# Kernel tuning notes

Measured on AMD Instinct MI355X. Metric: run time of the kernel, lower is better.

## Reference

```python
import jax, jax.numpy as jnp
import numpy as np

B, N, T, W, H, ED, S, C, E = 16, 256, 64, 12, 64, 64, 5, 4, 2048
ALPHA = 1.0
FG = W + H  # gcn_in_channels = window_size + tgcn_hidden_dim


def setup_inputs() -> dict:
    key = jax.random.key(0)
    ks = jax.random.split(key, 26)
    rn = lambda k, shape: jax.random.normal(k, shape, jnp.float32) * 0.1
    x = jax.random.normal(ks[0], (B, N, T), jnp.float32)
    src = jax.random.randint(ks[1], (E,), 0, N)
    off = jax.random.randint(ks[2], (E,), 1, N)
    dst = (src + off) % N  # no self loops
    return {
        'x': x,
        'static_edge_weight': jax.random.uniform(ks[3], (E,), jnp.float32),
        'gsl_gconv_w': rn(ks[4], (FG, ED)), 'gsl_gconv_b': rn(ks[5], (ED,)),
        'gsl_w1': rn(ks[6], (ED, ED)), 'gsl_b1': rn(ks[7], (ED,)),
        'gsl_w2': rn(ks[8], (ED, ED)), 'gsl_b2': rn(ks[9], (ED,)),
        'wz_c': rn(ks[10], (1, H)), 'bz_c': rn(ks[11], (H,)),
        'wz_l': rn(ks[12], (2 * H, H)), 'bz_l': rn(ks[13], (H,)),
        'wr_c': rn(ks[14], (1, H)), 'br_c': rn(ks[15], (H,)),
        'wr_l': rn(ks[16], (2 * H, H)), 'br_l': rn(ks[17], (H,)),
        'wh_c': rn(ks[18], (1, H)), 'bh_c': rn(ks[19], (H,)),
        'wh_l': rn(ks[20], (2 * H, H)), 'bh_l': rn(ks[21], (H,)),
        'cls_w': rn(ks[22], (N * H, C)), 'cls_b': rn(ks[23], (C,)),
        'static_edge_index': jnp.stack([src, dst]).astype(jnp.int32),
    }


def _normalize(A):
    # GCN sym-norm with added self loops; A has zero diagonal by construction.
    Ahat = A + jnp.eye(N, dtype=A.dtype)
    deg = Ahat.sum(axis=-2)  # in-degree (PyG gcn_norm scatters weight on col)
    dinv = jnp.where(deg > 0, 1.0 / jnp.sqrt(deg), 0.0)
    return dinv[..., :, None] * Ahat * dinv[..., None, :]


def reference(x, static_edge_weight, gsl_gconv_w, gsl_gconv_b, gsl_w1, gsl_b1,
              gsl_w2, gsl_b2, wz_c, bz_c, wz_l, bz_l, wr_c, br_c, wr_l, br_l,
              wh_c, bh_c, wh_l, bh_l, cls_w, cls_b, static_edge_index):
    A_stat = jnp.zeros((N, N), jnp.float32).at[static_edge_index[0], static_edge_index[1]].add(static_edge_weight)
    An_stat = _normalize(A_stat)  # [N,N]

    # Sliding windows, left-padded with zeros to window_size W.
    xp = jnp.pad(x, ((0, 0), (0, 0), (W - 1, 0)))
    widx = jnp.arange(T)[:, None] + jnp.arange(W)[None, :]
    wins = jnp.transpose(xp[:, :, widx], (2, 0, 1, 3))      # [T,B,N,W]
    xts = jnp.transpose(x, (2, 0, 1))[..., None]            # [T,B,N,1]
    cnts = jnp.minimum(jnp.arange(T) + 1, S).astype(jnp.float32)
    idxs = jnp.arange(T) % S

    def gcn_s(X, Wm, b):  # static graph, out[j] = sum_i Anorm[i,j] (XW)[i]
        return jnp.einsum('ij,bif->bjf', An_stat, X @ Wm) + b

    def gcn_d(An, X, Wm, b):  # per-batch dynamic graph
        return jnp.einsum('bij,bif->bjf', An, X @ Wm) + b

    def step(carry, xs):
        h, Eh = carry
        win, xt, cnt, idx = xs
        It = jnp.concatenate([win, h], axis=-1)             # [B,N,W+H]
        df = gcn_s(It, gsl_gconv_w, gsl_gconv_b)
        de1 = jnp.tanh(ALPHA * (df @ gsl_w1 + gsl_b1))
        de2 = jnp.tanh(ALPHA * (df @ gsl_w2 + gsl_b2))
        M12 = jnp.einsum('bie,bje->bij', de1, de2)          # de1 @ de2^T
        Et = jax.nn.relu(jnp.tanh(ALPHA * (M12 - jnp.swapaxes(M12, -1, -2))))
        Eh = Eh.at[:, idx].set(Et)                          # ring buffer write
        Mt = Eh.sum(axis=1) / cnt                           # mean over filled slots
        An = _normalize(Mt)
        cz = gcn_d(An, xt, wz_c, bz_c)
        z = jax.nn.sigmoid(jnp.concatenate([cz, h], -1) @ wz_l + bz_l)
        cr = gcn_d(An, xt, wr_c, br_c)
        r = jax.nn.sigmoid(jnp.concatenate([cr, h], -1) @ wr_l + br_l)
        ch = gcn_d(An, xt, wh_c, bh_c)
        ht = jnp.tanh(jnp.concatenate([ch, h * r], -1) @ wh_l + bh_l)
        h = z * h + (1.0 - z) * ht
        return (h, Eh), None

    h0 = jnp.zeros((B, N, H), jnp.float32)
    Eh0 = jnp.zeros((B, S, N, N), jnp.float32)
    (hT, _), _ = jax.lax.scan(step, (h0, Eh0), (wins, xts, cnts, idxs))
    return hT.reshape(B, N * H) @ cls_w + cls_b
```

## Files before the change

### kernel.cpp

```cpp
#include <hip/hip_runtime.h>
#include <hip/hip_bf16.h>


typedef unsigned short u16;
typedef unsigned int u32;
typedef unsigned long long u64;
typedef __attribute__((ext_vector_type(8))) short bf16x8;
typedef __attribute__((ext_vector_type(4))) float f32x4;

#define B_ 16
#define N_ 256
#define T_ 64
#define W_ 12
#define S_ 5
#define E_ 2048
#define G_ 16

__device__ __forceinline__ float b2f(u16 u) {
  union { u32 i; float f; } v; v.i = ((u32)u) << 16; return v.f;
}
__device__ __forceinline__ u16 f2b(float f) {
  union { float f; u32 i; } v; v.f = f;
  u32 x = v.i; x += 0x7fff + ((x >> 16) & 1); return (u16)(x >> 16);
}
__device__ __forceinline__ float ftanh(float x) {
  float e = __expf(-2.f * fabsf(x));
  float t = (1.f - e) / (1.f + e);
  return x < 0.f ? -t : t;
}
__device__ __forceinline__ float fsigm(float x) { return 1.f / (1.f + __expf(-x)); }
__device__ __forceinline__ float cvload(const void* p, size_t i, int f) {
  return f ? ((const float*)p)[i] : b2f(((const u16*)p)[i]);
}
__device__ __forceinline__ u16 cvloadb(const void* p, size_t i, int f) {
  return f ? f2b(((const float*)p)[i]) : ((const u16*)p)[i];
}
__device__ __forceinline__ float gld(const float* p) {
  return __hip_atomic_load(p, __ATOMIC_RELAXED, __HIP_MEMORY_SCOPE_SYSTEM);
}
__device__ __forceinline__ void gst(float* p, float v) {
  __hip_atomic_store(p, v, __ATOMIC_RELAXED, __HIP_MEMORY_SCOPE_SYSTEM);
}
__device__ __forceinline__ u64 gld64(const u64* p) {
  return __hip_atomic_load(p, __ATOMIC_RELAXED, __HIP_MEMORY_SCOPE_SYSTEM);
}
__device__ __forceinline__ void gst64(u64* p, u64 v) {
  __hip_atomic_store(p, v, __ATOMIC_RELAXED, __HIP_MEMORY_SCOPE_SYSTEM);
}
__device__ __forceinline__ u32 gldu(const u32* p) {
  return __hip_atomic_load(p, __ATOMIC_RELAXED, __HIP_MEMORY_SCOPE_SYSTEM);
}
__device__ __forceinline__ f32x4 mfma16(bf16x8 a, bf16x8 b, f32x4 c) {
  return __builtin_amdgcn_mfma_f32_16x16x32_bf16(a, b, c, 0, 0, 0);
}
__device__ __forceinline__ bf16x8 ldfrag(const u16* p) { return *(const bf16x8*)p; }

struct Params {
  const void *x0, *ew0, *gw0, *gb0, *w10, *b10, *w20, *b20;
  const void *wzc0, *bzc0, *wzl0, *bzl0, *wrc0, *brc0, *wrl0, *brl0;
  const void *whc0, *bhc0, *whl0, *bhl0, *clsw0, *clsb0;
  const int* eidx;
  float *Eh, *clspart;
  u64 *degsum, *de1g, *de2g, *xTp, *hgpT;
  u32 *tags;
  void* out;
};

__device__ __forceinline__ void wtag(const u32* tg, u32 target) {
  const int k = threadIdx.x & 15;
  while (!__all((int)(gldu(&tg[k]) >= target)))
    __builtin_amdgcn_s_sleep(1);
}
__device__ __forceinline__ void wtag8(const u32* tg, int base, u32 target) {
  const int k = base + (threadIdx.x & 7);
  while (!__all((int)(gldu(&tg[k]) >= target)))
    __builtin_amdgcn_s_sleep(1);
}
__device__ __forceinline__ void ptag(u32* tg, int wg, u32 val) {
  if (threadIdx.x == 0)
    __hip_atomic_store(&tg[wg], val, __ATOMIC_RELAXED, __HIP_MEMORY_SCOPE_SYSTEM);
}

__global__ void __launch_bounds__(256, 1) dtgcn_main(Params p) {
  __shared__ __align__(16) u16 s_union[21120];
  __shared__ __align__(16) u16 s_gwF[64 * 104];
  __shared__ __align__(16) u16 s_w1T[64 * 72], s_w2T[64 * 72];
  __shared__ __align__(16) u16 s_gzT[64 * 72], s_grT[64 * 72], s_ghT[64 * 72];
  __shared__ __align__(16) u16 s_antO1[16 * 264], s_antO2[16 * 264];
  __shared__ __align__(16) u16 s_m1[16 * 104];
  __shared__ float s_msum[16 * 257];
  __shared__ __align__(16) u16 s_de1I[16 * 72], s_de2I[16 * 72];
  __shared__ __align__(16) u16 s_hbf[16 * 72];
  __shared__ __align__(16) u16 s_dfhr[16 * 72];
  __shared__ float s_colv[16], s_degacc[16];
  __shared__ float s_y[256], s_dinv[256], s_s[16];
  __shared__ float s_uv[384], s_gb[64], s_b1[64], s_b2[64];
  __shared__ int s_flag;

  const int b = blockIdx.x & 15;
  const int wg = blockIdx.x >> 4;
  const int tid = threadIdx.x;
  const int lane = tid & 63;
  const int wv = tid >> 6;
  const int l = lane & 15;
  const int quad = lane >> 4;
  const int r0 = wg * 16;

  u64* de1g = p.de1g + (size_t)b * N_ * 16;
  u64* de2g = p.de2g + (size_t)b * N_ * 16;
  u64* hgpb = p.hgpT + (size_t)b * 64 * 64;
  u64* xTw  = p.xTp + (size_t)b * 64 * 64;
  const u64* xTb = xTw;
  u64* degb = p.degsum + (size_t)b * N_;
  u32* tgDe = p.tags + b * 128;
  u32* tgH  = p.tags + b * 128 + 32;
  u32* tgX  = p.tags + b * 128 + 48;
  u32* tgC  = p.tags + b * 128 + 64;

  if (tid == 0) {
    const u16* q = (const u16*)p.x0;
    int c = 0;
    for (int i = 0; i < 256; ++i) {
      int ex = (q[i] >> 7) & 0xff;
      c += (ex >= 110 && ex <= 135);
    }
    s_flag = (c < 200) ? 1 : 0;
  }
  __syncthreads();
  const int fl = s_flag;

  {
    u16* xs = s_union;
    #pragma unroll
    for (int r = 0; r < 4; ++r) {
      const int tt = wg * 4 + r;
      xs[r * 256 + tid] = f2b(cvload(p.x0, ((size_t)b * N_ + tid) * T_ + tt, fl));
    }
    __syncthreads();
    const int r = tid >> 6, c = tid & 63;
    u64 v = (u64)xs[r * 256 + 4 * c]
          | ((u64)xs[r * 256 + 4 * c + 1] << 16)
          | ((u64)xs[r * 256 + 4 * c + 2] << 32)
          | ((u64)xs[r * 256 + 4 * c + 3] << 48);
    gst64(&xTw[(size_t)(wg * 4 + r) * 64 + c], v);
    __syncthreads();
    ptag(tgX, wg, 1);
  }

  {
    float* s_acol = (float*)s_union;
    float* s_dg   = (float*)s_union + 4096;
    for (int i = tid; i < 4096; i += 256) s_acol[i] = 0.f;
    s_dg[tid] = 0.f;
    __syncthreads();
    for (int e2 = tid; e2 < E_; e2 += 256) {
      const int sN = p.eidx[e2], dN = p.eidx[E_ + e2];
      const float wv2 = cvload(p.ew0, e2, fl);
      atomicAdd(&s_dg[dN], wv2);
      const int dl = dN - r0;
      if (dl >= 0 && dl < 16) atomicAdd(&s_acol[sN * 16 + dl], wv2);
    }
    __syncthreads();
    s_dg[tid] = rsqrtf(1.f + s_dg[tid]);
    __syncthreads();
    for (int idx = tid; idx < 4096; idx += 256) {
      const int jl = idx >> 8, i = idx & 255;
      float a = s_acol[i * 16 + jl] + ((i == r0 + jl) ? 1.f : 0.f);
      float v = s_dg[i] * a * s_dg[r0 + jl];
      u16 hi = f2b(v);
      s_antO1[jl * 264 + i] = hi;
      s_antO2[jl * 264 + i] = f2b(v - b2f(hi));
    }
  }

  for (int idx = tid; idx < 64 * 104; idx += 256) {
    const int ee = idx / 104, k = idx - ee * 104;
    u16 v = 0;
    if (k < 64) v = cvloadb(p.gw0, (12 + k) * 64 + ee, fl);
    else if (k < 76) v = cvloadb(p.gw0, (k - 64) * 64 + ee, fl);
    s_gwF[ee * 104 + k] = v;
  }
  for (int idx = tid; idx < 4096; idx += 256) {
    const int ee = idx >> 6, ff = idx & 63;
    s_w1T[ee * 72 + ff] = cvloadb(p.w10, ff * 64 + ee, fl);
    s_w2T[ee * 72 + ff] = cvloadb(p.w20, ff * 64 + ee, fl);
    s_gzT[ee * 72 + ff] = cvloadb(p.wzl0, 4096 + ff * 64 + ee, fl);
    s_grT[ee * 72 + ff] = cvloadb(p.wrl0, 4096 + ff * 64 + ee, fl);
    s_ghT[ee * 72 + ff] = cvloadb(p.whl0, 4096 + ff * 64 + ee, fl);
  }
  if (tid < 64) {
    const int e2 = tid;
    float uz = 0, vz = 0, ur = 0, vr = 0, uh = 0, vh = 0;
    for (int f = 0; f < 64; ++f) {
      float wz = cvload(p.wzl0, f * 64 + e2, fl);
      float wr = cvload(p.wrl0, f * 64 + e2, fl);
      float wh = cvload(p.whl0, f * 64 + e2, fl);
      uz += cvload(p.wzc0, f, fl) * wz; vz += cvload(p.bzc0, f, fl) * wz;
      ur += cvload(p.wrc0, f, fl) * wr; vr += cvload(p.brc0, f, fl) * wr;
      uh += cvload(p.whc0, f, fl) * wh; vh += cvload(p.bhc0, f, fl) * wh;
    }
    s_uv[0 * 64 + e2] = uz; s_uv[1 * 64 + e2] = vz + cvload(p.bzl0, e2, fl);
    s_uv[2 * 64 + e2] = ur; s_uv[3 * 64 + e2] = vr + cvload(p.brl0, e2, fl);
    s_uv[4 * 64 + e2] = uh; s_uv[5 * 64 + e2] = vh + cvload(p.bhl0, e2, fl);
    s_gb[tid] = cvload(p.gb0, tid, fl);
    s_b1[tid] = cvload(p.b10, tid, fl);
    s_b2[tid] = cvload(p.b20, tid, fl);
  }
  for (int idx = tid; idx < 16 * 257; idx += 256) s_msum[idx] = 0.f;
  for (int idx = tid; idx < 16 * 72; idx += 256) s_hbf[idx] = 0;
  for (int idx = tid; idx < 16 * 104; idx += 256) s_m1[idx] = 0;
  for (int idx = 20064 + tid; idx < 21120; idx += 256) s_union[idx] = 0;
  if (tid < 16) s_degacc[tid] = 0.f;
  __syncthreads();

  u16* s_itT = s_union;
  u16* s_j1  = s_union;
  u16* s_j2  = s_union + 9216;

  float hreg[4] = {0.f, 0.f, 0.f, 0.f};
  const int e = wv * 16 + l;

  for (int t = 0; t < T_; ++t) {
    float xv;
    {
      if (t == 0) wtag(tgX, 1);
      xv = cvload(p.x0, ((size_t)b * N_ + tid) * T_ + t, fl);
      u64 tw0[2], tw1[2];
      #pragma unroll
      for (int q = 0; q < 2; ++q) {
        const int idx = q * 256 + tid;
        const int row = idx >> 5, c = idx & 31;
        const bool ok = idx < 384;
        const int tx = t - (W_ - 1) + row;
        const bool live = ok && tx >= 0;
        tw0[q] = live ? gld64(&xTb[(size_t)tx * 64 + c]) : 0ull;
        tw1[q] = live ? gld64(&xTb[(size_t)tx * 64 + 32 + c]) : 0ull;
      }
      wtag8(tgH, 0, (u32)t);
      {
        u64 th[8];
        #pragma unroll
        for (int q = 0; q < 8; ++q) {
          const int idx = q * 256 + tid;
          const int row = idx >> 5, c = idx & 31;
          th[q] = gld64(&hgpb[(size_t)row * 64 + c]);
        }
        #pragma unroll
        for (int q = 0; q < 8; ++q) {
          const int idx = q * 256 + tid;
          const int row = idx >> 5, c = idx & 31;
          *(u64*)&s_itT[row * 264 + c * 4] = th[q];
        }
        #pragma unroll
        for (int q = 0; q < 2; ++q) {
          const int idx = q * 256 + tid;
          if (idx < 384) {
            const int row = idx >> 5, c = idx & 31;
            *(u64*)&s_itT[(64 + row) * 264 + c * 4] = tw0[q];
          }
        }
      }
      __syncthreads();
      wtag8(tgH, 8, (u32)t);
      u64 th1[8];
      #pragma unroll
      for (int q = 0; q < 8; ++q) {
        const int idx = q * 256 + tid;
        const int row = idx >> 5, c = idx & 31;
        th1[q] = gld64(&hgpb[(size_t)row * 64 + 32 + c]);
      }
      f32x4 accA[2];
      accA[0] = (f32x4){0.f, 0.f, 0.f, 0.f};
      accA[1] = (f32x4){0.f, 0.f, 0.f, 0.f};
      {
        int ti = 0;
        for (int nt = wv; nt < 5; nt += 4, ++ti) {
          #pragma unroll
          for (int ch = 0; ch < 4; ++ch) {
            const int io = ch * 32 + quad * 8;
            bf16x8 bfr = ldfrag(&s_itT[(nt * 16 + l) * 264 + io]);
            accA[ti] = mfma16(ldfrag(&s_antO1[l * 264 + io]), bfr, accA[ti]);
            accA[ti] = mfma16(ldfrag(&s_antO2[l * 264 + io]), bfr, accA[ti]);
          }
        }
      }
      #pragma unroll
      for (int q = 0; q < 8; ++q) {
        const int idx = q * 256 + tid;
        const int row = idx >> 5, c = idx & 31;
        *(u64*)&s_itT[row * 264 + (32 + c) * 4] = th1[q];
      }
      #pragma unroll
      for (int q = 0; q < 2; ++q) {
        const int idx = q * 256 + tid;
        if (idx < 384) {
          const int row = idx >> 5, c = idx & 31;
          *(u64*)&s_itT[(64 + row) * 264 + (32 + c) * 4] = tw1[q];
        }
      }
      __syncthreads();
      {
        int ti = 0;
        for (int nt = wv; nt < 5; nt += 4, ++ti) {
          #pragma unroll
          for (int ch = 4; ch < 8; ++ch) {
            const int io = ch * 32 + quad * 8;
            bf16x8 bfr = ldfrag(&s_itT[(nt * 16 + l) * 264 + io]);
            accA[ti] = mfma16(ldfrag(&s_antO1[l * 264 + io]), bfr, accA[ti]);
            accA[ti] = mfma16(ldfrag(&s_antO2[l * 264 + io]), bfr, accA[ti]);
          }
          #pragma unroll
          for (int r = 0; r < 4; ++r)
            s_m1[(quad * 4 + r) * 104 + nt * 16 + l] = f2b(accA[ti][r]);
        }
      }
      __syncthreads();
      {
        f32x4 dfa = {0.f, 0.f, 0.f, 0.f};
        #pragma unroll
        for (int ks = 0; ks < 3; ++ks) {
          bf16x8 afr = ldfrag(&s_m1[l * 104 + ks * 32 + quad * 8]);
          dfa = mfma16(afr, ldfrag(&s_gwF[e * 104 + ks * 32 + quad * 8]), dfa);
        }
        #pragma unroll
        for (int r = 0; r < 4; ++r)
          s_dfhr[(quad * 4 + r) * 72 + e] = f2b(dfa[r] + s_gb[e]);
      }
      __syncthreads();
      {
        f32x4 E1, E2;
        #pragma unroll
        for (int r = 0; r < 4; ++r) { E1[r] = s_b1[e]; E2[r] = s_b2[e]; }
        #pragma unroll
        for (int ks = 0; ks < 2; ++ks) {
          bf16x8 afr = ldfrag(&s_dfhr[l * 72 + ks * 32 + quad * 8]);
          E1 = mfma16(afr, ldfrag(&s_w1T[e * 72 + ks * 32 + quad * 8]), E1);
          E2 = mfma16(afr, ldfrag(&s_w2T[e * 72 + ks * 32 + quad * 8]), E2);
        }
        u32 v1[4], v2[4];
        #pragma unroll
        for (int r = 0; r < 4; ++r) {
          v1[r] = (u32)f2b(ftanh(E1[r]));
          v2[r] = (u32)f2b(ftanh(E2[r]));
          s_de1I[(quad * 4 + r) * 72 + e] = (u16)v1[r];
          s_de2I[(quad * 4 + r) * 72 + e] = (u16)v2[r];
        }
        #pragma unroll
        for (int r = 0; r < 4; ++r) {
          u32 a1 = (u32)__shfl_xor((int)v1[r], 1);
          u32 a2 = (u32)__shfl_xor((int)v2[r], 1);
          u32 ev1 = (l & 1) ? a1 : v1[r], od1 = (l & 1) ? v1[r] : a1;
          u32 ev2 = (l & 1) ? a2 : v2[r], od2 = (l & 1) ? v2[r] : a2;
          u32 w1 = ev1 | (od1 << 16), w2 = ev2 | (od2 << 16);
          u32 x1 = (u32)__shfl_xor((int)w1, 2);
          u32 x2 = (u32)__shfl_xor((int)w2, 2);
          u64 q1 = (l & 2) ? ((u64)x1 | ((u64)w1 << 32)) : ((u64)w1 | ((u64)x1 << 32));
          u64 q2 = (l & 2) ? ((u64)x2 | ((u64)w2 << 32)) : ((u64)w2 | ((u64)x2 << 32));
          if ((l & 3) == 0) {
            const size_t ro = (size_t)(r0 + quad * 4 + r) * 16 + wv * 4 + (l >> 2);
            gst64(&de1g[ro], q1);
            gst64(&de2g[ro], q2);
          }
        }
      }
      __syncthreads();
      ptag(tgDe, wg, (u32)(t + 1));
    }

    {
      const int sidx = t % S_;
      float* Ehc = p.Eh + ((size_t)((b * S_ + sidx) * G_ + wg)) * (N_ * 16);
      if (tid < 16) s_colv[tid] = 0.f;
      bf16x8 bq1[2], bq2[2];
      #pragma unroll
      for (int ks = 0; ks < 2; ++ks) {
        bq1[ks] = ldfrag(&s_de1I[l * 72 + ks * 32 + quad * 8]);
        bq2[ks] = ldfrag(&s_de2I[l * 72 + ks * 32 + quad * 8]);
      }
      const int havold = (t >= S_);
      float old0[2][4] = {{0.f, 0.f, 0.f, 0.f}, {0.f, 0.f, 0.f, 0.f}};
      float old1[2][4] = {{0.f, 0.f, 0.f, 0.f}, {0.f, 0.f, 0.f, 0.f}};
      if (havold) {
        #pragma unroll
        for (int mt2 = 0; mt2 < 2; ++mt2) {
          const int mt = wv * 2 + mt2;
          #pragma unroll
          for (int r = 0; r < 4; ++r) {
            const int i0 = mt * 16 + quad * 4 + r;
            old0[mt2][r] = Ehc[(size_t)i0 * 16 + l];
            old1[mt2][r] = Ehc[(size_t)(128 + i0) * 16 + l];
          }
        }
      }
      const u32 dtgt = (u32)(t + 1);
      wtag8(tgDe, 0, dtgt);
      u64 t1a[8], t2a[8];
      #pragma unroll
      for (int q = 0; q < 8; ++q) {
        const int idx = q * 256 + tid;
        const int row = idx >> 4, c = idx & 15;
        t1a[q] = gld64(&de1g[(size_t)row * 16 + c]);
        t2a[q] = gld64(&de2g[(size_t)row * 16 + c]);
      }
      #pragma unroll
      for (int q = 0; q < 8; ++q) {
        const int idx = q * 256 + tid;
        const int row = idx >> 4, c = idx & 15;
        *(u64*)&s_j1[row * 72 + c * 4] = t1a[q];
        *(u64*)&s_j2[row * 72 + c * 4] = t2a[q];
      }
      __syncthreads();
      wtag8(tgDe, 8, dtgt);
      u64 t1b[8], t2b[8];
      #pragma unroll
      for (int q = 0; q < 8; ++q) {
        const int idx = q * 256 + tid;
        const int row = idx >> 4, c = idx & 15;
        t1b[q] = gld64(&de1g[(size_t)(128 + row) * 16 + c]);
        t2b[q] = gld64(&de2g[(size_t)(128 + row) * 16 + c]);
      }
      float dcacc = 0.f;
      #pragma unroll
      for (int mt2 = 0; mt2 < 2; ++mt2) {
        const int mt = wv * 2 + mt2;
        f32x4 D1 = {0.f, 0.f, 0.f, 0.f}, D2 = {0.f, 0.f, 0.f, 0.f};
        #pragma unroll
        for (int ks = 0; ks < 2; ++ks) {
          bf16x8 a1 = ldfrag(&s_j1[(mt * 16 + l) * 72 + ks * 32 + quad * 8]);
          bf16x8 a2 = ldfrag(&s_j2[(mt * 16 + l) * 72 + ks * 32 + quad * 8]);
          D1 = mfma16(a1, bq2[ks], D1);
          D2 = mfma16(a2, bq1[ks], D2);
        }
        #pragma unroll
        for (int r = 0; r < 4; ++r) {
          const int i = mt * 16 + quad * 4 + r;
          float d = ftanh(D1[r] - D2[r]);
          float eN = fmaxf(d, 0.f);
          float dd = eN - old0[mt2][r];
          Ehc[(size_t)i * 16 + l] = eN;
          s_msum[l * 257 + i] += dd;
          dcacc += dd;
        }
      }
      __syncthreads();
      #pragma unroll
      for (int q = 0; q < 8; ++q) {
        const int idx = q * 256 + tid;
        const int row = idx >> 4, c = idx & 15;
        *(u64*)&s_j1[row * 72 + c * 4] = t1b[q];
        *(u64*)&s_j2[row * 72 + c * 4] = t2b[q];
      }
      __syncthreads();
      #pragma unroll
      for (int mt2 = 0; mt2 < 2; ++mt2) {
        const int mt = wv * 2 + mt2;
        f32x4 D1 = {0.f, 0.f, 0.f, 0.f}, D2 = {0.f, 0.f, 0.f, 0.f};
        #pragma unroll
        for (int ks = 0; ks < 2; ++ks) {
          bf16x8 a1 = ldfrag(&s_j1[(mt * 16 + l) * 72 + ks * 32 + quad * 8]);
          bf16x8 a2 = ldfrag(&s_j2[(mt * 16 + l) * 72 + ks * 32 + quad * 8]);
          D1 = mfma16(a1, bq2[ks], D1);
          D2 = mfma16(a2, bq1[ks], D2);
        }
        #pragma unroll
        for (int r = 0; r < 4; ++r) {
          const int i = 128 + mt * 16 + quad * 4 + r;
          float d = ftanh(D1[r] - D2[r]);
          float eN = fmaxf(d, 0.f);
          float dd = eN - old1[mt2][r];
          Ehc[(size_t)i * 16 + l] = eN;
          s_msum[l * 257 + i] += dd;
          dcacc += dd;
        }
      }
      dcacc += __shfl_xor(dcacc, 16);
      dcacc += __shfl_xor(dcacc, 32);
      if (lane < 16) atomicAdd(&s_colv[lane], dcacc);
      __syncthreads();
      if (tid < 16) {
        float nd = s_degacc[tid] + s_colv[tid];
        s_degacc[tid] = nd;
        union { float f; u32 i; } cv; cv.f = nd;
        gst64(&degb[r0 + tid], (u64)cv.i | ((u64)dtgt << 32));
      }
    }

    {
      f32x4 azh = {0.f, 0.f, 0.f, 0.f}, arh = {0.f, 0.f, 0.f, 0.f};
      #pragma unroll
      for (int ks = 0; ks < 2; ++ks) {
        bf16x8 afr = ldfrag(&s_hbf[l * 72 + ks * 32 + quad * 8]);
        azh = mfma16(afr, ldfrag(&s_gzT[e * 72 + ks * 32 + quad * 8]), azh);
        arh = mfma16(afr, ldfrag(&s_grT[e * 72 + ks * 32 + quad * 8]), arh);
      }
      const u32 dgt = (u32)(t + 1);
      u64 du;
      for (;;) {
        du = gld64(&degb[tid]);
        if (__all((int)((u32)(du >> 32) >= dgt))) break;
        __builtin_amdgcn_s_sleep(1);
      }
      const float cnt = (float)((t + 1 < S_) ? (t + 1) : S_);
      const float invc = 1.f / cnt;
      {
        union { u32 i; float f; } dv; dv.i = (u32)du;
        float dg = 1.f + dv.f * invc;
        float di = rsqrtf(dg);
        s_dinv[tid] = di;
        s_y[tid] = di * xv;
      }
      __syncthreads();
      {
        const int jl = tid >> 4, cc = tid & 15;
        float part = 0.f;
        #pragma unroll
        for (int k = 0; k < 16; ++k) {
          const int i = cc * 16 + ((k + cc) & 15);
          part += s_msum[jl * 257 + i] * s_y[i];
        }
        part += __shfl_xor(part, 1);
        part += __shfl_xor(part, 2);
        part += __shfl_xor(part, 4);
        part += __shfl_xor(part, 8);
        if (cc == 0) {
          const int j = r0 + jl;
          s_s[jl] = s_dinv[j] * (part * invc + s_y[j]);
        }
      }
      __syncthreads();
      float sv[4];
      #pragma unroll
      for (int r = 0; r < 4; ++r) sv[r] = s_s[quad * 4 + r];
      float zz[4], rr2[4];
      #pragma unroll
      for (int r = 0; r < 4; ++r) {
        zz[r]  = fsigm(azh[r] + s_uv[0 * 64 + e] * sv[r] + s_uv[1 * 64 + e]);
        rr2[r] = fsigm(arh[r] + s_uv[2 * 64 + e] * sv[r] + s_uv[3 * 64 + e]);
      }
      #pragma unroll
      for (int r = 0; r < 4; ++r)
        s_dfhr[(quad * 4 + r) * 72 + e] = f2b(hreg[r] * rr2[r]);
      __syncthreads();
      f32x4 ah;
      #pragma unroll
      for (int r = 0; r < 4; ++r) ah[r] = s_uv[4 * 64 + e] * sv[r] + s_uv[5 * 64 + e];
      #pragma unroll
      for (int ks = 0; ks < 2; ++ks) {
        bf16x8 afr = ldfrag(&s_dfhr[l * 72 + ks * 32 + quad * 8]);
        ah = mfma16(afr, ldfrag(&s_ghT[e * 72 + ks * 32 + quad * 8]), ah);
      }
      #pragma unroll
      for (int r = 0; r < 4; ++r) {
        float ht = ftanh(ah[r]);
        hreg[r] = zz[r] * hreg[r] + (1.f - zz[r]) * ht;
      }
      {
        u16 h0 = f2b(hreg[0]), h1 = f2b(hreg[1]);
        u16 h2 = f2b(hreg[2]), h3 = f2b(hreg[3]);
        u64 hv = (u64)h0 | ((u64)h1 << 16) | ((u64)h2 << 32) | ((u64)h3 << 48);
        gst64(&hgpb[(size_t)e * 64 + (r0 >> 2) + quad], hv);
        s_hbf[(quad * 4 + 0) * 72 + e] = h0;
        s_hbf[(quad * 4 + 1) * 72 + e] = h1;
        s_hbf[(quad * 4 + 2) * 72 + e] = h2;
        s_hbf[(quad * 4 + 3) * 72 + e] = h3;
      }
      __syncthreads();
      ptag(tgH, wg, (u32)(t + 1));
    }
  }

  {
    float part[4] = {0.f, 0.f, 0.f, 0.f};
    #pragma unroll
    for (int r = 0; r < 4; ++r) {
      const size_t base = ((size_t)(r0 + quad * 4 + r) * 64 + e) * 4;
      #pragma unroll
      for (int c = 0; c < 4; ++c)
        part[c] += hreg[r] * cvload(p.clsw0, base + c, fl);
    }
    #pragma unroll
    for (int c = 0; c < 4; ++c) {
      float v = part[c];
      v += __shfl_xor(v, 1);  v += __shfl_xor(v, 2);
      v += __shfl_xor(v, 4);  v += __shfl_xor(v, 8);
      v += __shfl_xor(v, 16); v += __shfl_xor(v, 32);
      if (lane == 0) s_s[wv * 4 + c] = v;
    }
    __syncthreads();
    if (tid < 4) {
      float tot = s_s[0 + tid] + s_s[4 + tid] + s_s[8 + tid] + s_s[12 + tid];
      gst(&p.clspart[(b * 16 + wg) * 4 + tid], tot);
    }
    __syncthreads();
    ptag(tgC, wg, 1);
    if (wg == 0) {
      wtag(tgC, 1);
      if (tid < 4) {
        float v = 0.f;
        for (int k = 0; k < 16; ++k) v += gld(&p.clspart[(b * 16 + k) * 4 + tid]);
        v += cvload(p.clsb0, tid, fl);
        if (fl) ((float*)p.out)[b * 4 + tid] = v;
        else    ((u16*)p.out)[b * 4 + tid] = f2b(v);
      }
    }
  }
}

extern "C" void kernel_launch(void* const* d_in, const int* in_sizes, int n_in,
                              void* d_out, int out_size, void* d_ws, size_t ws_size,
                              hipStream_t stream) {
  float* w = (float*)d_ws;
  size_t o = 0;
  auto alloc = [&](size_t n) { float* r = w + o; o += (n + 63) & ~(size_t)63; return r; };
  u64* xTp  = (u64*)alloc((size_t)B_ * 64 * 128);
  float* clspart = alloc(B_ * 16 * 4);
  u64* de1g = (u64*)alloc((size_t)B_ * N_ * 32);
  u64* de2g = (u64*)alloc((size_t)B_ * N_ * 32);
  float* Eh = alloc((size_t)B_ * S_ * N_ * N_);
  const size_t zero_off = o;
  u64*   hgpT  = (u64*)alloc((size_t)B_ * 64 * 128);
  u64*   degs  = (u64*)alloc((size_t)B_ * N_ * 2);
  u32*   tags  = (u32*)alloc(B_ * 128);
  if (ws_size < o * sizeof(float)) return;

  (void)hipMemsetAsync(w + zero_off, 0, (o - zero_off) * sizeof(float), stream);

  Params p;
  p.x0  = d_in[0];  p.ew0 = d_in[1];
  p.gw0 = d_in[2];  p.gb0 = d_in[3];
  p.w10 = d_in[4];  p.b10 = d_in[5];
  p.w20 = d_in[6];  p.b20 = d_in[7];
  p.wzc0 = d_in[8];  p.bzc0 = d_in[9];  p.wzl0 = d_in[10]; p.bzl0 = d_in[11];
  p.wrc0 = d_in[12]; p.brc0 = d_in[13]; p.wrl0 = d_in[14]; p.brl0 = d_in[15];
  p.whc0 = d_in[16]; p.bhc0 = d_in[17]; p.whl0 = d_in[18]; p.bhl0 = d_in[19];
  p.clsw0 = d_in[20]; p.clsb0 = d_in[21];
  p.eidx = (const int*)d_in[22];
  p.Eh = Eh; p.clspart = clspart;
  p.degsum = degs;
  p.de1g = de1g; p.de2g = de2g; p.xTp = xTp; p.hgpT = hgpT;
  p.tags = tags; p.out = d_out;

  void* args[] = { &p };
  hipError_t ce = hipLaunchCooperativeKernel((const void*)dtgcn_main,
                                             dim3(B_ * G_), dim3(256), args, 0, stream);
  if (ce != hipSuccess) {
    (void)hipGetLastError();
    dtgcn_main<<<dim3(B_ * G_), dim3(256), 0, stream>>>(p);
  }
}
```

Measured before the change: 870.4 us.

## Load MFMA operands directly from global and use per-wave readiness flags

The global h/x and de1/de2 operands are now loaded straight into MFMA fragments in registers instead of being staged through shared memory. This removes several __syncthreads barriers and the shared staging buffer. Readiness tags become per-wave (4 per workgroup, wtag32 polling 32 flags) and each wave publishes its own flag after a vmcnt wait, instead of a block barrier followed by a single flag store. This cuts intra-block synchronisation on the serial time loop, at the cost of more polled flags, uncoalesced 8-byte global loads and the correctness burden of relaxed-atomic ordering.

```diff
diff --git a/kernel.cpp b/kernel.cpp
--- a/kernel.cpp
+++ b/kernel.cpp
@@ -54,6 +54,9 @@
   return __builtin_amdgcn_mfma_f32_16x16x32_bf16(a, b, c, 0, 0, 0);
 }
 __device__ __forceinline__ bf16x8 ldfrag(const u16* p) { return *(const bf16x8*)p; }
+__device__ __forceinline__ bf16x8 mkfrag(u64 lo, u64 hi) {
+  union { u64 q[2]; bf16x8 v; } u; u.q[0] = lo; u.q[1] = hi; return u.v;
+}
 
 struct Params {
   const void *x0, *ew0, *gw0, *gb0, *w10, *b10, *w20, *b20;
@@ -71,8 +74,8 @@
   while (!__all((int)(gldu(&tg[k]) >= target)))
     __builtin_amdgcn_s_sleep(1);
 }
-__device__ __forceinline__ void wtag8(const u32* tg, int base, u32 target) {
-  const int k = base + (threadIdx.x & 7);
+__device__ __forceinline__ void wtag32(const u32* tg, int base, u32 target) {
+  const int k = base + (threadIdx.x & 31);
   while (!__all((int)(gldu(&tg[k]) >= target)))
     __builtin_amdgcn_s_sleep(1);
 }
@@ -80,9 +83,14 @@
   if (threadIdx.x == 0)
     __hip_atomic_store(&tg[wg], val, __ATOMIC_RELAXED, __HIP_MEMORY_SCOPE_SYSTEM);
 }
+__device__ __forceinline__ void ptagw(u32* tg, int slot, u32 val) {
+  asm volatile("s_waitcnt vmcnt(0)" ::: "memory");
+  if ((threadIdx.x & 63) == 0)
+    __hip_atomic_store(&tg[slot], val, __ATOMIC_RELAXED, __HIP_MEMORY_SCOPE_SYSTEM);
+}
 
 __global__ void __launch_bounds__(256, 1) dtgcn_main(Params p) {
-  __shared__ __align__(16) u16 s_union[21120];
+  __shared__ __align__(16) u16 s_union[8704];
   __shared__ __align__(16) u16 s_gwF[64 * 104];
   __shared__ __align__(16) u16 s_w1T[64 * 72], s_w2T[64 * 72];
   __shared__ __align__(16) u16 s_gzT[64 * 72], s_grT[64 * 72], s_ghT[64 * 72];
@@ -112,10 +120,10 @@
   u64* xTw  = p.xTp + (size_t)b * 64 * 64;
   const u64* xTb = xTw;
   u64* degb = p.degsum + (size_t)b * N_;
-  u32* tgDe = p.tags + b * 128;
-  u32* tgH  = p.tags + b * 128 + 32;
-  u32* tgX  = p.tags + b * 128 + 48;
-  u32* tgC  = p.tags + b * 128 + 64;
+  u32* tgDe4 = p.tags + b * 256;
+  u32* tgH4  = p.tags + b * 256 + 64;
+  u32* tgX   = p.tags + b * 256 + 128;
+  u32* tgC   = p.tags + b * 256 + 144;
 
   if (tid == 0) {
     const u16* q = (const u16*)p.x0;
@@ -209,13 +217,8 @@
   for (int idx = tid; idx < 16 * 257; idx += 256) s_msum[idx] = 0.f;
   for (int idx = tid; idx < 16 * 72; idx += 256) s_hbf[idx] = 0;
   for (int idx = tid; idx < 16 * 104; idx += 256) s_m1[idx] = 0;
-  for (int idx = 20064 + tid; idx < 21120; idx += 256) s_union[idx] = 0;
   if (tid < 16) s_degacc[tid] = 0.f;
   __syncthreads();
-
-  u16* s_itT = s_union;
-  u16* s_j1  = s_union;
-  u16* s_j2  = s_union + 9216;
 
   float hreg[4] = {0.f, 0.f, 0.f, 0.f};
   const int e = wv * 16 + l;
@@ -225,94 +228,53 @@
     {
       if (t == 0) wtag(tgX, 1);
       xv = cvload(p.x0, ((size_t)b * N_ + tid) * T_ + t, fl);
-      u64 tw0[2], tw1[2];
-      #pragma unroll
-      for (int q = 0; q < 2; ++q) {
-        const int idx = q * 256 + tid;
-        const int row = idx >> 5, c = idx & 31;
-        const bool ok = idx < 384;
-        const int tx = t - (W_ - 1) + row;
-        const bool live = ok && tx >= 0;
-        tw0[q] = live ? gld64(&xTb[(size_t)tx * 64 + c]) : 0ull;
-        tw1[q] = live ? gld64(&xTb[(size_t)tx * 64 + 32 + c]) : 0ull;
-      }
-      wtag8(tgH, 0, (u32)t);
-      {
-        u64 th[8];
-        #pragma unroll
-        for (int q = 0; q < 8; ++q) {
-          const int idx = q * 256 + tid;
-          const int row = idx >> 5, c = idx & 31;
-          th[q] = gld64(&hgpb[(size_t)row * 64 + c]);
-        }
-        #pragma unroll
-        for (int q = 0; q < 8; ++q) {
-          const int idx = q * 256 + tid;
-          const int row = idx >> 5, c = idx & 31;
-          *(u64*)&s_itT[row * 264 + c * 4] = th[q];
-        }
-        #pragma unroll
-        for (int q = 0; q < 2; ++q) {
-          const int idx = q * 256 + tid;
-          if (idx < 384) {
-            const int row = idx >> 5, c = idx & 31;
-            *(u64*)&s_itT[(64 + row) * 264 + c * 4] = tw0[q];
-          }
-        }
-      }
-      __syncthreads();
-      wtag8(tgH, 8, (u32)t);
-      u64 th1[8];
-      #pragma unroll
-      for (int q = 0; q < 8; ++q) {
-        const int idx = q * 256 + tid;
-        const int row = idx >> 5, c = idx & 31;
-        th1[q] = gld64(&hgpb[(size_t)row * 64 + 32 + c]);
-      }
-      f32x4 accA[2];
-      accA[0] = (f32x4){0.f, 0.f, 0.f, 0.f};
-      accA[1] = (f32x4){0.f, 0.f, 0.f, 0.f};
-      {
-        int ti = 0;
-        for (int nt = wv; nt < 5; nt += 4, ++ti) {
-          #pragma unroll
-          for (int ch = 0; ch < 4; ++ch) {
-            const int io = ch * 32 + quad * 8;
-            bf16x8 bfr = ldfrag(&s_itT[(nt * 16 + l) * 264 + io]);
-            accA[ti] = mfma16(ldfrag(&s_antO1[l * 264 + io]), bfr, accA[ti]);
-            accA[ti] = mfma16(ldfrag(&s_antO2[l * 264 + io]), bfr, accA[ti]);
-          }
-        }
-      }
-      #pragma unroll
-      for (int q = 0; q < 8; ++q) {
-        const int idx = q * 256 + tid;
-        const int row = idx >> 5, c = idx & 31;
-        *(u64*)&s_itT[row * 264 + (32 + c) * 4] = th1[q];
-      }
-      #pragma unroll
-      for (int q = 0; q < 2; ++q) {
-        const int idx = q * 256 + tid;
-        if (idx < 384) {
-          const int row = idx >> 5, c = idx & 31;
-          *(u64*)&s_itT[(64 + row) * 264 + (32 + c) * 4] = tw1[q];
-        }
-      }
-      __syncthreads();
-      {
-        int ti = 0;
-        for (int nt = wv; nt < 5; nt += 4, ++ti) {
-          #pragma unroll
-          for (int ch = 4; ch < 8; ++ch) {
-            const int io = ch * 32 + quad * 8;
-            bf16x8 bfr = ldfrag(&s_itT[(nt * 16 + l) * 264 + io]);
-            accA[ti] = mfma16(ldfrag(&s_antO1[l * 264 + io]), bfr, accA[ti]);
-            accA[ti] = mfma16(ldfrag(&s_antO2[l * 264 + io]), bfr, accA[ti]);
-          }
-          #pragma unroll
-          for (int r = 0; r < 4; ++r)
-            s_m1[(quad * 4 + r) * 104 + nt * 16 + l] = f2b(accA[ti][r]);
-        }
+      u64 b2l[8][2];
+      if (wv == 0) {
+        const int tx = t - (W_ - 1) + l;
+        const bool live = (l < W_) && (tx >= 0);
+        #pragma unroll
+        for (int ch = 0; ch < 8; ++ch) {
+          b2l[ch][0] = live ? gld64(&xTb[(size_t)tx * 64 + ch * 8 + quad * 2]) : 0ull;
+          b2l[ch][1] = live ? gld64(&xTb[(size_t)tx * 64 + ch * 8 + quad * 2 + 1]) : 0ull;
+        }
+      }
+      const u32 htgt = (u32)t;
+      u64 b1l[8][2];
+      wtag32(tgH4, 0, htgt);
+      #pragma unroll
+      for (int ch = 0; ch < 4; ++ch) {
+        b1l[ch][0] = gld64(&hgpb[(size_t)e * 64 + ch * 8 + quad * 2]);
+        b1l[ch][1] = gld64(&hgpb[(size_t)e * 64 + ch * 8 + quad * 2 + 1]);
+      }
+      wtag32(tgH4, 32, htgt);
+      #pragma unroll
+      for (int ch = 4; ch < 8; ++ch) {
+        b1l[ch][0] = gld64(&hgpb[(size_t)e * 64 + ch * 8 + quad * 2]);
+        b1l[ch][1] = gld64(&hgpb[(size_t)e * 64 + ch * 8 + quad * 2 + 1]);
+      }
+      f32x4 acc0 = {0.f, 0.f, 0.f, 0.f};
+      #pragma unroll
+      for (int ch = 0; ch < 8; ++ch) {
+        bf16x8 bfr = mkfrag(b1l[ch][0], b1l[ch][1]);
+        const int io = ch * 32 + quad * 8;
+        acc0 = mfma16(ldfrag(&s_antO1[l * 264 + io]), bfr, acc0);
+        acc0 = mfma16(ldfrag(&s_antO2[l * 264 + io]), bfr, acc0);
+      }
+      #pragma unroll
+      for (int r = 0; r < 4; ++r)
+        s_m1[(quad * 4 + r) * 104 + e] = f2b(acc0[r]);
+      if (wv == 0) {
+        f32x4 acc1 = {0.f, 0.f, 0.f, 0.f};
+        #pragma unroll
+        for (int ch = 0; ch < 8; ++ch) {
+          bf16x8 bfr = mkfrag(b2l[ch][0], b2l[ch][1]);
+          const int io = ch * 32 + quad * 8;
+          acc1 = mfma16(ldfrag(&s_antO1[l * 264 + io]), bfr, acc1);
+          acc1 = mfma16(ldfrag(&s_antO2[l * 264 + io]), bfr, acc1);
+        }
+        #pragma unroll
+        for (int r = 0; r < 4; ++r)
+          s_m1[(quad * 4 + r) * 104 + 64 + l] = f2b(acc1[r]);
       }
       __syncthreads();
       {
@@ -363,14 +325,14 @@
           }
         }
       }
-      __syncthreads();
-      ptag(tgDe, wg, (u32)(t + 1));
+      ptagw(tgDe4, wg * 4 + wv, (u32)(t + 1));
+      if (tid < 16) s_colv[tid] = 0.f;
+      __syncthreads();
     }
 
     {
       const int sidx = t % S_;
       float* Ehc = p.Eh + ((size_t)((b * S_ + sidx) * G_ + wg)) * (N_ * 16);
-      if (tid < 16) s_colv[tid] = 0.f;
       bf16x8 bq1[2], bq2[2];
       #pragma unroll
       for (int ks = 0; ks < 2; ++ks) {
@@ -393,31 +355,31 @@
         }
       }
       const u32 dtgt = (u32)(t + 1);
-      wtag8(tgDe, 0, dtgt);
-      u64 t1a[8], t2a[8];
-      #pragma unroll
-      for (int q = 0; q < 8; ++q) {
-        const int idx = q * 256 + tid;
-        const int row = idx >> 4, c = idx & 15;
-        t1a[q] = gld64(&de1g[(size_t)row * 16 + c]);
-        t2a[q] = gld64(&de2g[(size_t)row * 16 + c]);
-      }
-      #pragma unroll
-      for (int q = 0; q < 8; ++q) {
-        const int idx = q * 256 + tid;
-        const int row = idx >> 4, c = idx & 15;
-        *(u64*)&s_j1[row * 72 + c * 4] = t1a[q];
-        *(u64*)&s_j2[row * 72 + c * 4] = t2a[q];
-      }
-      __syncthreads();
-      wtag8(tgDe, 8, dtgt);
-      u64 t1b[8], t2b[8];
-      #pragma unroll
-      for (int q = 0; q < 8; ++q) {
-        const int idx = q * 256 + tid;
-        const int row = idx >> 4, c = idx & 15;
-        t1b[q] = gld64(&de1g[(size_t)(128 + row) * 16 + c]);
-        t2b[q] = gld64(&de2g[(size_t)(128 + row) * 16 + c]);
+      wtag32(tgDe4, 0, dtgt);
+      u64 a1[2][2][2], a2[2][2][2];
+      #pragma unroll
+      for (int mt2 = 0; mt2 < 2; ++mt2) {
+        const size_t row = (size_t)((wv * 2 + mt2) * 16 + l);
+        #pragma unroll
+        for (int ks = 0; ks < 2; ++ks) {
+          a1[mt2][ks][0] = gld64(&de1g[row * 16 + ks * 8 + quad * 2]);
+          a1[mt2][ks][1] = gld64(&de1g[row * 16 + ks * 8 + quad * 2 + 1]);
+          a2[mt2][ks][0] = gld64(&de2g[row * 16 + ks * 8 + quad * 2]);
+          a2[mt2][ks][1] = gld64(&de2g[row * 16 + ks * 8 + quad * 2 + 1]);
+        }
+      }
+      wtag32(tgDe4, 32, dtgt);
+      u64 c1[2][2][2], c2[2][2][2];
+      #pragma unroll
+      for (int mt2 = 0; mt2 < 2; ++mt2) {
+        const size_t row = (size_t)(128 + (wv * 2 + mt2) * 16 + l);
+        #pragma unroll
+        for (int ks = 0; ks < 2; ++ks) {
+          c1[mt2][ks][0] = gld64(&de1g[row * 16 + ks * 8 + quad * 2]);
+          c1[mt2][ks][1] = gld64(&de1g[row * 16 + ks * 8 + quad * 2 + 1]);
+          c2[mt2][ks][0] = gld64(&de2g[row * 16 + ks * 8 + quad * 2]);
+          c2[mt2][ks][1] = gld64(&de2g[row * 16 + ks * 8 + quad * 2 + 1]);
+        }
       }
       float dcacc = 0.f;
       #pragma unroll
@@ -426,10 +388,8 @@
         f32x4 D1 = {0.f, 0.f, 0.f, 0.f}, D2 = {0.f, 0.f, 0.f, 0.f};
         #pragma unroll
         for (int ks = 0; ks < 2; ++ks) {
-          bf16x8 a1 = ldfrag(&s_j1[(mt * 16 + l) * 72 + ks * 32 + quad * 8]);
-          bf16x8 a2 = ldfrag(&s_j2[(mt * 16 + l) * 72 + ks * 32 + quad * 8]);
-          D1 = mfma16(a1, bq2[ks], D1);
-          D2 = mfma16(a2, bq1[ks], D2);
+          D1 = mfma16(mkfrag(a1[mt2][ks][0], a1[mt2][ks][1]), bq2[ks], D1);
+          D2 = mfma16(mkfrag(a2[mt2][ks][0], a2[mt2][ks][1]), bq1[ks], D2);
         }
         #pragma unroll
         for (int r = 0; r < 4; ++r) {
@@ -442,25 +402,14 @@
           dcacc += dd;
         }
       }
-      __syncthreads();
-      #pragma unroll
-      for (int q = 0; q < 8; ++q) {
-        const int idx = q * 256 + tid;
-        const int row = idx >> 4, c = idx & 15;
-        *(u64*)&s_j1[row * 72 + c * 4] = t1b[q];
-        *(u64*)&s_j2[row * 72 + c * 4] = t2b[q];
-      }
-      __syncthreads();
       #pragma unroll
       for (int mt2 = 0; mt2 < 2; ++mt2) {
         const int mt = wv * 2 + mt2;
         f32x4 D1 = {0.f, 0.f, 0.f, 0.f}, D2 = {0.f, 0.f, 0.f, 0.f};
         #pragma unroll
         for (int ks = 0; ks < 2; ++ks) {
-          bf16x8 a1 = ldfrag(&s_j1[(mt * 16 + l) * 72 + ks * 32 + quad * 8]);
-          bf16x8 a2 = ldfrag(&s_j2[(mt * 16 + l) * 72 + ks * 32 + quad * 8]);
-          D1 = mfma16(a1, bq2[ks], D1);
-          D2 = mfma16(a2, bq1[ks], D2);
+          D1 = mfma16(mkfrag(c1[mt2][ks][0], c1[mt2][ks][1]), bq2[ks], D1);
+          D2 = mfma16(mkfrag(c2[mt2][ks][0], c2[mt2][ks][1]), bq1[ks], D2);
         }
         #pragma unroll
         for (int r = 0; r < 4; ++r) {
@@ -564,8 +513,7 @@
         s_hbf[(quad * 4 + 2) * 72 + e] = h2;
         s_hbf[(quad * 4 + 3) * 72 + e] = h3;
       }
-      __syncthreads();
-      ptag(tgH, wg, (u32)(t + 1));
+      ptagw(tgH4, wg * 4 + wv, (u32)(t + 1));
     }
   }
 
@@ -620,7 +568,7 @@
   const size_t zero_off = o;
   u64*   hgpT  = (u64*)alloc((size_t)B_ * 64 * 128);
   u64*   degs  = (u64*)alloc((size_t)B_ * N_ * 2);
-  u32*   tags  = (u32*)alloc(B_ * 128);
+  u32*   tags  = (u32*)alloc(B_ * 256);
   if (ws_size < o * sizeof(float)) return;
 
   (void)hipMemsetAsync(w + zero_off, 0, (o - zero_off) * sizeof(float), stream);
```

Measured after the change: 1.341 ms. 1.54x slower.

## Reassociate GCN as An·(It·Wg), exchange projected features instead of raw inputs

Applied to the files above, without the earlier changes.

The graph convolution on [window, h] is reassociated from (An·It)·Wg to An·(It·Wg). Each workgroup now projects its own 16 rows of the window and hidden state through the GCN weight locally and publishes only that 64-wide projection. The old path broadcast the transposed x windows and the hidden state and ran a two-stage matmul through an intermediate buffer. This removes the xT publishing phase, the extra tile pass in the adjacency matmul and the s_m1 staging, and merges two cross-workgroup tag channels into one. Spin waits also gain a bounded iteration cap, which risks returning before the data is ready, and the product is rounded to bf16 before the adjacency multiply, which changes numerics slightly.

```diff
diff --git a/kernel.cpp b/kernel.cpp
--- a/kernel.cpp
+++ b/kernel.cpp
@@ -15,6 +15,7 @@
 #define S_ 5
 #define E_ 2048
 #define G_ 16
+#define SPIN_MAX (1u << 20)
 
 __device__ __forceinline__ float b2f(u16 u) {
   union { u32 i; float f; } v; v.i = ((u32)u) << 16; return v.f;
@@ -61,20 +62,24 @@
   const void *whc0, *bhc0, *whl0, *bhl0, *clsw0, *clsb0;
   const int* eidx;
   float *Eh, *clspart;
-  u64 *degsum, *de1g, *de2g, *xTp, *hgpT;
+  u64 *degsum, *de1g, *de2g, *Ggp;
   u32 *tags;
   void* out;
 };
 
 __device__ __forceinline__ void wtag(const u32* tg, u32 target) {
   const int k = threadIdx.x & 15;
-  while (!__all((int)(gldu(&tg[k]) >= target)))
+  for (u32 s = 0; s < SPIN_MAX; ++s) {
+    if (__all((int)(gldu(&tg[k]) >= target))) return;
     __builtin_amdgcn_s_sleep(1);
+  }
 }
 __device__ __forceinline__ void wtag8(const u32* tg, int base, u32 target) {
   const int k = base + (threadIdx.x & 7);
-  while (!__all((int)(gldu(&tg[k]) >= target)))
+  for (u32 s = 0; s < SPIN_MAX; ++s) {
+    if (__all((int)(gldu(&tg[k]) >= target))) return;
     __builtin_amdgcn_s_sleep(1);
+  }
 }
 __device__ __forceinline__ void ptag(u32* tg, int wg, u32 val) {
   if (threadIdx.x == 0)
@@ -82,12 +87,13 @@
 }
 
 __global__ void __launch_bounds__(256, 1) dtgcn_main(Params p) {
-  __shared__ __align__(16) u16 s_union[21120];
-  __shared__ __align__(16) u16 s_gwF[64 * 104];
+  __shared__ __align__(16) u16 s_union[18432];
+  __shared__ __align__(16) u16 s_gwHT[64 * 72];
+  __shared__ __align__(16) u16 s_gwWT[64 * 32];
+  __shared__ __align__(16) u16 s_xw[16 * 96];
   __shared__ __align__(16) u16 s_w1T[64 * 72], s_w2T[64 * 72];
   __shared__ __align__(16) u16 s_gzT[64 * 72], s_grT[64 * 72], s_ghT[64 * 72];
   __shared__ __align__(16) u16 s_antO1[16 * 264], s_antO2[16 * 264];
-  __shared__ __align__(16) u16 s_m1[16 * 104];
   __shared__ float s_msum[16 * 257];
   __shared__ __align__(16) u16 s_de1I[16 * 72], s_de2I[16 * 72];
   __shared__ __align__(16) u16 s_hbf[16 * 72];
@@ -108,14 +114,11 @@
 
   u64* de1g = p.de1g + (size_t)b * N_ * 16;
   u64* de2g = p.de2g + (size_t)b * N_ * 16;
-  u64* hgpb = p.hgpT + (size_t)b * 64 * 64;
-  u64* xTw  = p.xTp + (size_t)b * 64 * 64;
-  const u64* xTb = xTw;
+  u64* Ggp  = p.Ggp + (size_t)b * 64 * 64;
   u64* degb = p.degsum + (size_t)b * N_;
-  u32* tgDe = p.tags + b * 128;
-  u32* tgH  = p.tags + b * 128 + 32;
-  u32* tgX  = p.tags + b * 128 + 48;
-  u32* tgC  = p.tags + b * 128 + 64;
+  u32* tgDe = p.tags + b * 64;
+  u32* tgG  = p.tags + b * 64 + 16;
+  u32* tgC  = p.tags + b * 64 + 32;
 
   if (tid == 0) {
     const u16* q = (const u16*)p.x0;
@@ -128,24 +131,6 @@
   }
   __syncthreads();
   const int fl = s_flag;
-
-  {
-    u16* xs = s_union;
-    #pragma unroll
-    for (int r = 0; r < 4; ++r) {
-      const int tt = wg * 4 + r;
-      xs[r * 256 + tid] = f2b(cvload(p.x0, ((size_t)b * N_ + tid) * T_ + tt, fl));
-    }
-    __syncthreads();
-    const int r = tid >> 6, c = tid & 63;
-    u64 v = (u64)xs[r * 256 + 4 * c]
-          | ((u64)xs[r * 256 + 4 * c + 1] << 16)
-          | ((u64)xs[r * 256 + 4 * c + 2] << 32)
-          | ((u64)xs[r * 256 + 4 * c + 3] << 48);
-    gst64(&xTw[(size_t)(wg * 4 + r) * 64 + c], v);
-    __syncthreads();
-    ptag(tgX, wg, 1);
-  }
 
   {
     float* s_acol = (float*)s_union;
@@ -173,12 +158,20 @@
     }
   }
 
-  for (int idx = tid; idx < 64 * 104; idx += 256) {
-    const int ee = idx / 104, k = idx - ee * 104;
-    u16 v = 0;
-    if (k < 64) v = cvloadb(p.gw0, (12 + k) * 64 + ee, fl);
-    else if (k < 76) v = cvloadb(p.gw0, (k - 64) * 64 + ee, fl);
-    s_gwF[ee * 104 + k] = v;
+  for (int idx = tid; idx < 64 * 72; idx += 256) {
+    const int ee = idx / 72, k = idx - ee * 72;
+    s_gwHT[idx] = (k < 64) ? cvloadb(p.gw0, (12 + k) * 64 + ee, fl) : (u16)0;
+  }
+  for (int idx = tid; idx < 64 * 32; idx += 256) {
+    const int ee = idx >> 5, w2 = idx & 31;
+    s_gwWT[idx] = (w2 < 12) ? cvloadb(p.gw0, w2 * 64 + ee, fl) : (u16)0;
+  }
+  for (int idx = tid; idx < 16 * 96; idx += 256) {
+    const int i = idx / 96, u = idx - i * 96;
+    const int tt = u - (W_ - 1);
+    s_xw[idx] = (tt >= 0 && tt < T_)
+                ? f2b(cvload(p.x0, ((size_t)b * N_ + r0 + i) * T_ + tt, fl))
+                : (u16)0;
   }
   for (int idx = tid; idx < 4096; idx += 256) {
     const int ee = idx >> 6, ff = idx & 63;
@@ -208,124 +201,85 @@
   }
   for (int idx = tid; idx < 16 * 257; idx += 256) s_msum[idx] = 0.f;
   for (int idx = tid; idx < 16 * 72; idx += 256) s_hbf[idx] = 0;
-  for (int idx = tid; idx < 16 * 104; idx += 256) s_m1[idx] = 0;
-  for (int idx = 20064 + tid; idx < 21120; idx += 256) s_union[idx] = 0;
   if (tid < 16) s_degacc[tid] = 0.f;
   __syncthreads();
 
-  u16* s_itT = s_union;
-  u16* s_j1  = s_union;
-  u16* s_j2  = s_union + 9216;
+  const int e = wv * 16 + l;
+
+  {
+    union { u16 a[8]; bf16x8 v; } ux;
+    #pragma unroll
+    for (int j = 0; j < 8; ++j) ux.a[j] = s_xw[l * 96 + quad * 8 + j];
+    f32x4 g = mfma16(ux.v, ldfrag(&s_gwWT[e * 32 + quad * 8]),
+                     (f32x4){0.f, 0.f, 0.f, 0.f});
+    u64 gv = (u64)f2b(g[0]) | ((u64)f2b(g[1]) << 16)
+           | ((u64)f2b(g[2]) << 32) | ((u64)f2b(g[3]) << 48);
+    gst64(&Ggp[(size_t)e * 64 + (r0 >> 2) + quad], gv);
+    __syncthreads();
+    ptag(tgG, wg, 1);
+  }
+
+  u16* s_gT = s_union;
+  u16* s_j1 = s_union;
+  u16* s_j2 = s_union + 9216;
 
   float hreg[4] = {0.f, 0.f, 0.f, 0.f};
-  const int e = wv * 16 + l;
 
   for (int t = 0; t < T_; ++t) {
     float xv;
     {
-      if (t == 0) wtag(tgX, 1);
       xv = cvload(p.x0, ((size_t)b * N_ + tid) * T_ + t, fl);
-      u64 tw0[2], tw1[2];
-      #pragma unroll
-      for (int q = 0; q < 2; ++q) {
-        const int idx = q * 256 + tid;
-        const int row = idx >> 5, c = idx & 31;
-        const bool ok = idx < 384;
-        const int tx = t - (W_ - 1) + row;
-        const bool live = ok && tx >= 0;
-        tw0[q] = live ? gld64(&xTb[(size_t)tx * 64 + c]) : 0ull;
-        tw1[q] = live ? gld64(&xTb[(size_t)tx * 64 + 32 + c]) : 0ull;
-      }
-      wtag8(tgH, 0, (u32)t);
+      const u32 gtgt = (u32)(t + 1);
+      wtag8(tgG, 0, gtgt);
       {
         u64 th[8];
         #pragma unroll
         for (int q = 0; q < 8; ++q) {
           const int idx = q * 256 + tid;
           const int row = idx >> 5, c = idx & 31;
-          th[q] = gld64(&hgpb[(size_t)row * 64 + c]);
+          th[q] = gld64(&Ggp[(size_t)row * 64 + c]);
         }
         #pragma unroll
         for (int q = 0; q < 8; ++q) {
           const int idx = q * 256 + tid;
           const int row = idx >> 5, c = idx & 31;
-          *(u64*)&s_itT[row * 264 + c * 4] = th[q];
-        }
-        #pragma unroll
-        for (int q = 0; q < 2; ++q) {
-          const int idx = q * 256 + tid;
-          if (idx < 384) {
-            const int row = idx >> 5, c = idx & 31;
-            *(u64*)&s_itT[(64 + row) * 264 + c * 4] = tw0[q];
-          }
-        }
-      }
-      __syncthreads();
-      wtag8(tgH, 8, (u32)t);
+          *(u64*)&s_gT[row * 264 + c * 4] = th[q];
+        }
+      }
+      __syncthreads();
+      wtag8(tgG, 8, gtgt);
       u64 th1[8];
       #pragma unroll
       for (int q = 0; q < 8; ++q) {
         const int idx = q * 256 + tid;
         const int row = idx >> 5, c = idx & 31;
-        th1[q] = gld64(&hgpb[(size_t)row * 64 + 32 + c]);
-      }
-      f32x4 accA[2];
-      accA[0] = (f32x4){0.f, 0.f, 0.f, 0.f};
-      accA[1] = (f32x4){0.f, 0.f, 0.f, 0.f};
-      {
-        int ti = 0;
-        for (int nt = wv; nt < 5; nt += 4, ++ti) {
-          #pragma unroll
-          for (int ch = 0; ch < 4; ++ch) {
-            const int io = ch * 32 + quad * 8;
-            bf16x8 bfr = ldfrag(&s_itT[(nt * 16 + l) * 264 + io]);
-            accA[ti] = mfma16(ldfrag(&s_antO1[l * 264 + io]), bfr, accA[ti]);
-            accA[ti] = mfma16(ldfrag(&s_antO2[l * 264 + io]), bfr, accA[ti]);
-          }
-        }
+        th1[q] = gld64(&Ggp[(size_t)row * 64 + 32 + c]);
+      }
+      f32x4 dfa = {0.f, 0.f, 0.f, 0.f};
+      #pragma unroll
+      for (int ch = 0; ch < 4; ++ch) {
+        const int io = ch * 32 + quad * 8;
+        bf16x8 bfr = ldfrag(&s_gT[e * 264 + io]);
+        dfa = mfma16(ldfrag(&s_antO1[l * 264 + io]), bfr, dfa);
+        dfa = mfma16(ldfrag(&s_antO2[l * 264 + io]), bfr, dfa);
       }
       #pragma unroll
       for (int q = 0; q < 8; ++q) {
         const int idx = q * 256 + tid;
         const int row = idx >> 5, c = idx & 31;
-        *(u64*)&s_itT[row * 264 + (32 + c) * 4] = th1[q];
-      }
-      #pragma unroll
-      for (int q = 0; q < 2; ++q) {
-        const int idx = q * 256 + tid;
-        if (idx < 384) {
-          const int row = idx >> 5, c = idx & 31;
-          *(u64*)&s_itT[(64 + row) * 264 + (32 + c) * 4] = tw1[q];
-        }
-      }
-      __syncthreads();
-      {
-        int ti = 0;
-        for (int nt = wv; nt < 5; nt += 4, ++ti) {
-          #pragma unroll
-          for (int ch = 4; ch < 8; ++ch) {
-            const int io = ch * 32 + quad * 8;
-            bf16x8 bfr = ldfrag(&s_itT[(nt * 16 + l) * 264 + io]);
-            accA[ti] = mfma16(ldfrag(&s_antO1[l * 264 + io]), bfr, accA[ti]);
-            accA[ti] = mfma16(ldfrag(&s_antO2[l * 264 + io]), bfr, accA[ti]);
-          }
-          #pragma unroll
-          for (int r = 0; r < 4; ++r)
-            s_m1[(quad * 4 + r) * 104 + nt * 16 + l] = f2b(accA[ti][r]);
-        }
-      }
-      __syncthreads();
-      {
-        f32x4 dfa = {0.f, 0.f, 0.f, 0.f};
-        #pragma unroll
-        for (int ks = 0; ks < 3; ++ks) {
-          bf16x8 afr = ldfrag(&s_m1[l * 104 + ks * 32 + quad * 8]);
-          dfa = mfma16(afr, ldfrag(&s_gwF[e * 104 + ks * 32 + quad * 8]), dfa);
-        }
-        #pragma unroll
-        for (int r = 0; r < 4; ++r)
-          s_dfhr[(quad * 4 + r) * 72 + e] = f2b(dfa[r] + s_gb[e]);
-      }
+        *(u64*)&s_gT[row * 264 + (32 + c) * 4] = th1[q];
+      }
+      __syncthreads();
+      #pragma unroll
+      for (int ch = 4; ch < 8; ++ch) {
+        const int io = ch * 32 + quad * 8;
+        bf16x8 bfr = ldfrag(&s_gT[e * 264 + io]);
+        dfa = mfma16(ldfrag(&s_antO1[l * 264 + io]), bfr, dfa);
+        dfa = mfma16(ldfrag(&s_antO2[l * 264 + io]), bfr, dfa);
+      }
+      #pragma unroll
+      for (int r = 0; r < 4; ++r)
+        s_dfhr[(quad * 4 + r) * 72 + e] = f2b(dfa[r] + s_gb[e]);
       __syncthreads();
       {
         f32x4 E1, E2;
@@ -494,8 +448,8 @@
         arh = mfma16(afr, ldfrag(&s_grT[e * 72 + ks * 32 + quad * 8]), arh);
       }
       const u32 dgt = (u32)(t + 1);
-      u64 du;
-      for (;;) {
+      u64 du = 0;
+      for (u32 sp = 0; sp < SPIN_MAX; ++sp) {
         du = gld64(&degb[tid]);
         if (__all((int)((u32)(du >> 32) >= dgt))) break;
         __builtin_amdgcn_s_sleep(1);
@@ -554,18 +508,28 @@
         float ht = ftanh(ah[r]);
         hreg[r] = zz[r] * hreg[r] + (1.f - zz[r]) * ht;
       }
+      s_hbf[(quad * 4 + 0) * 72 + e] = f2b(hreg[0]);
+      s_hbf[(quad * 4 + 1) * 72 + e] = f2b(hreg[1]);
+      s_hbf[(quad * 4 + 2) * 72 + e] = f2b(hreg[2]);
+      s_hbf[(quad * 4 + 3) * 72 + e] = f2b(hreg[3]);
+      __syncthreads();
       {
-        u16 h0 = f2b(hreg[0]), h1 = f2b(hreg[1]);
-        u16 h2 = f2b(hreg[2]), h3 = f2b(hreg[3]);
-        u64 hv = (u64)h0 | ((u64)h1 << 16) | ((u64)h2 << 32) | ((u64)h3 << 48);
-        gst64(&hgpb[(size_t)e * 64 + (r0 >> 2) + quad], hv);
-        s_hbf[(quad * 4 + 0) * 72 + e] = h0;
-        s_hbf[(quad * 4 + 1) * 72 + e] = h1;
-        s_hbf[(quad * 4 + 2) * 72 + e] = h2;
-        s_hbf[(quad * 4 + 3) * 72 + e] = h3;
-      }
-      __syncthreads();
-      ptag(tgH, wg, (u32)(t + 1));
+        union { u16 a[8]; bf16x8 v; } ux;
+        const int ub = (t + 1) + quad * 8;
+        #pragma unroll
+        for (int j = 0; j < 8; ++j) ux.a[j] = s_xw[l * 96 + ub + j];
+        f32x4 g = mfma16(ux.v, ldfrag(&s_gwWT[e * 32 + quad * 8]),
+                         (f32x4){0.f, 0.f, 0.f, 0.f});
+        #pragma unroll
+        for (int ks = 0; ks < 2; ++ks)
+          g = mfma16(ldfrag(&s_hbf[l * 72 + ks * 32 + quad * 8]),
+                     ldfrag(&s_gwHT[e * 72 + ks * 32 + quad * 8]), g);
+        u64 gv = (u64)f2b(g[0]) | ((u64)f2b(g[1]) << 16)
+               | ((u64)f2b(g[2]) << 32) | ((u64)f2b(g[3]) << 48);
+        gst64(&Ggp[(size_t)e * 64 + (r0 >> 2) + quad], gv);
+      }
+      __syncthreads();
+      ptag(tgG, wg, (u32)(t + 2));
     }
   }
 
@@ -612,15 +576,14 @@
   float* w = (float*)d_ws;
   size_t o = 0;
   auto alloc = [&](size_t n) { float* r = w + o; o += (n + 63) & ~(size_t)63; return r; };
-  u64* xTp  = (u64*)alloc((size_t)B_ * 64 * 128);
   float* clspart = alloc(B_ * 16 * 4);
   u64* de1g = (u64*)alloc((size_t)B_ * N_ * 32);
   u64* de2g = (u64*)alloc((size_t)B_ * N_ * 32);
+  u64* Ggp  = (u64*)alloc((size_t)B_ * 64 * 128);
   float* Eh = alloc((size_t)B_ * S_ * N_ * N_);
   const size_t zero_off = o;
-  u64*   hgpT  = (u64*)alloc((size_t)B_ * 64 * 128);
   u64*   degs  = (u64*)alloc((size_t)B_ * N_ * 2);
-  u32*   tags  = (u32*)alloc(B_ * 128);
+  u32*   tags  = (u32*)alloc(B_ * 64);
   if (ws_size < o * sizeof(float)) return;
 
   (void)hipMemsetAsync(w + zero_off, 0, (o - zero_off) * sizeof(float), stream);
@@ -637,7 +600,7 @@
   p.eidx = (const int*)d_in[22];
   p.Eh = Eh; p.clspart = clspart;
   p.degsum = degs;
-  p.de1g = de1g; p.de2g = de2g; p.xTp = xTp; p.hgpT = hgpT;
+  p.de1g = de1g; p.de2g = de2g; p.Ggp = Ggp;
   p.tags = tags; p.out = d_out;
 
   void* args[] = { &p };
```

Result: faster. 822.6 us (median of 3 runs) (-5.5%).
